# Kernel tuning notes

Hardware: AMD Instinct MI355X
Metric: run time of the kernel (lower is better)

## Reference

```python
import jax, jax.numpy as jnp
import numpy as np

B, L, D = 2, 2048, 2560
H, KV, HD = 8, 4, 256
FF = 10240
WINDOW = 1024
ROPE_BASE = 10000.0
EPS = 1e-6


def rmsnorm(x, scale=None):
    x32 = x.astype(jnp.float32)
    var = jnp.mean(jnp.square(x32), axis=-1, keepdims=True)
    xn = x32 * jax.lax.rsqrt(var + EPS)
    return xn if scale is None else xn * scale.astype(jnp.float32)


def apply_rope(x, positions, base):
    # full RoPE (rope_fraction=1.0): rotate pairs (i, i+head_dim//2)
    hd = x.shape[-1]
    half = hd // 2
    timescale = base ** (2.0 * jnp.arange(half, dtype=jnp.float32) / hd)
    ang = positions[:, :, None].astype(jnp.float32) / timescale  # [B,L,half]
    sin = jnp.sin(ang)[:, :, None, :]  # [B,L,1,half]
    cos = jnp.cos(ang)[:, :, None, :]
    x1, x2 = x[..., :half], x[..., half:]
    return jnp.concatenate([x1 * cos - x2 * sin, x2 * cos + x1 * sin], axis=-1)


def setup_inputs() -> dict:
    key = jax.random.key(0)
    ks = jax.random.split(key, 16)
    s = lambda fan_in: 1.0 / np.sqrt(fan_in)
    return {
        "x": jax.random.normal(ks[0], (B, L, D), jnp.float32),
        "positions": jnp.broadcast_to(jnp.arange(L, dtype=jnp.int32), (B, L)),
        "wq": jax.random.normal(ks[1], (D, H * HD), jnp.float32) * s(D),
        "wk": jax.random.normal(ks[2], (D, KV * HD), jnp.float32) * s(D),
        "wv": jax.random.normal(ks[3], (D, KV * HD), jnp.float32) * s(D),
        "wo": jax.random.normal(ks[4], (H * HD, D), jnp.float32) * s(H * HD),
        "q_scale": jnp.ones((HD,), jnp.float32),
        "k_scale": jnp.ones((HD,), jnp.float32),
        "pre_attn_scale": jnp.ones((D,), jnp.float32),
        "post_attn_scale": jnp.ones((D,), jnp.float32),
        "pre_ffw_scale": jnp.ones((D,), jnp.float32),
        "post_ffw_scale": jnp.ones((D,), jnp.float32),
        "w_gate": jax.random.normal(ks[5], (D, FF), jnp.float32) * s(D),
        "w_up": jax.random.normal(ks[6], (D, FF), jnp.float32) * s(D),
        "w_down": jax.random.normal(ks[7], (FF, D), jnp.float32) * s(FF),
    }


def reference(x, positions, wq, wk, wv, wo, q_scale, k_scale,
              pre_attn_scale, post_attn_scale, pre_ffw_scale, post_ffw_scale,
              w_gate, w_up, w_down):
    # --- attention sub-block ---
    h = rmsnorm(x, pre_attn_scale)
    q = (h @ wq).reshape(B, L, H, HD)
    k = (h @ wk).reshape(B, L, KV, HD)
    v = (h @ wv).reshape(B, L, KV, HD)
    q = apply_rope(rmsnorm(q, q_scale), positions, ROPE_BASE)
    k = apply_rope(rmsnorm(k, k_scale), positions, ROPE_BASE)
    v = rmsnorm(v)  # RMSNormNoScale on V
    rep = H // KV
    k = jnp.repeat(k, rep, axis=2)  # [B,L,H,HD]
    v = jnp.repeat(v, rep, axis=2)
    scores = jnp.einsum("bqhd,bkhd->bhqk", q, k)  # NOTE: no 1/sqrt(d) scaling, faithful to source
    i = jnp.arange(L)[:, None]
    j = jnp.arange(L)[None, :]
    mask = (j <= i) & (j > i - WINDOW)  # causal & sliding window
    scores = jnp.where(mask[None, None, :, :], scores, -10000.0)
    probs = jax.nn.softmax(scores.astype(jnp.float32), axis=-1)
    attn = jnp.einsum("bhqk,bkhd->bqhd", probs, v).reshape(B, L, H * HD)
    attn = attn @ wo
    x = x + rmsnorm(attn, post_attn_scale)
    # --- feedforward sub-block (GeGLU) ---
    h = rmsnorm(x, pre_ffw_scale)
    hidden = jax.nn.gelu(h @ w_gate, approximate=False) * (h @ w_up)
    ffw = hidden @ w_down
    x = x + rmsnorm(ffw, post_ffw_scale)
    return x
```

## Files before the change

kernel.cpp:

```cpp
#include <hip/hip_runtime.h>
#include <math.h>

#define DEV __device__ __forceinline__

typedef _Float16 f16;
typedef _Float16 f16x8 __attribute__((ext_vector_type(8)));
typedef _Float16 f16x4 __attribute__((ext_vector_type(4)));
typedef float f32x4 __attribute__((ext_vector_type(4)));

DEV void gload_lds16(const void* g, void* l) {
  __builtin_amdgcn_global_load_lds(
      (const __attribute__((address_space(1))) void*)g,
      (__attribute__((address_space(3))) void*)l, 16, 0, 0);
}

__global__ void transpose_w(const float* __restrict__ src, f16* __restrict__ dst,
                            int R, int C) {
  __shared__ float tile[32][33];
  int c0 = blockIdx.x * 32, r0 = blockIdx.y * 32;
  int tx = threadIdx.x, ty = threadIdx.y;
#pragma unroll
  for (int j = 0; j < 32; j += 8)
    tile[ty + j][tx] = src[(size_t)(r0 + ty + j) * C + c0 + tx];
  __syncthreads();
#pragma unroll
  for (int j = 0; j < 32; j += 8)
    dst[(size_t)(c0 + ty + j) * R + r0 + tx] = (f16)tile[tx][ty + j];
}

__global__ void rope_table_k(float* __restrict__ tab) {
  int idx = blockIdx.x * 256 + threadIdx.x;
  int pos = idx >> 7, j = idx & 127;
  float ts = powf(10000.0f, (float)j * (1.0f / 128.0f));
  float ang = (float)pos / ts;
  tab[pos * 256 + j] = sinf(ang);
  tab[pos * 256 + 128 + j] = cosf(ang);
}

__global__ __launch_bounds__(256) void rmsnorm_f32_f16(
    const float* __restrict__ in, const float* __restrict__ scale,
    f16* __restrict__ out) {
  constexpr int D = 2560, N4 = D / 4;
  const int m = blockIdx.x, tid = threadIdx.x;
  const float* row = in + (size_t)m * D;
  float vals[12];
  float ss = 0.f;
#pragma unroll
  for (int it = 0; it < 3; ++it) {
    int c4 = tid + it * 256;
    if (c4 < N4) {
      float4 v = *(const float4*)(row + c4 * 4);
      vals[it * 4 + 0] = v.x; vals[it * 4 + 1] = v.y;
      vals[it * 4 + 2] = v.z; vals[it * 4 + 3] = v.w;
      ss += v.x * v.x + v.y * v.y + v.z * v.z + v.w * v.w;
    }
  }
#pragma unroll
  for (int off = 32; off; off >>= 1) ss += __shfl_xor(ss, off, 64);
  __shared__ float red[4];
  if ((tid & 63) == 0) red[tid >> 6] = ss;
  __syncthreads();
  float rs = rsqrtf((red[0] + red[1] + red[2] + red[3]) * (1.0f / D) + 1e-6f);
#pragma unroll
  for (int it = 0; it < 3; ++it) {
    int c4 = tid + it * 256;
    if (c4 < N4) {
      float4 sc = *(const float4*)(scale + c4 * 4);
      f16x4 o;
      o[0] = (f16)(vals[it * 4 + 0] * rs * sc.x);
      o[1] = (f16)(vals[it * 4 + 1] * rs * sc.y);
      o[2] = (f16)(vals[it * 4 + 2] * rs * sc.z);
      o[3] = (f16)(vals[it * 4 + 3] * rs * sc.w);
      *(f16x4*)(out + (size_t)m * D + c4 * 4) = o;
    }
  }
}

__global__ __launch_bounds__(256) void residual_rmsnorm(
    const float* x, const f16* __restrict__ y,
    const float* __restrict__ scale, float* out) {
  constexpr int D = 2560, N4 = D / 4;
  const int m = blockIdx.x, tid = threadIdx.x;
  const f16* yr = y + (size_t)m * D;
  float yv[12];
  float ss = 0.f;
#pragma unroll
  for (int it = 0; it < 3; ++it) {
    int c4 = tid + it * 256;
    if (c4 < N4) {
      f16x4 u = *(const f16x4*)(yr + c4 * 4);
      float a = (float)u[0], b = (float)u[1], c = (float)u[2], d = (float)u[3];
      yv[it * 4 + 0] = a; yv[it * 4 + 1] = b; yv[it * 4 + 2] = c; yv[it * 4 + 3] = d;
      ss += a * a + b * b + c * c + d * d;
    }
  }
#pragma unroll
  for (int off = 32; off; off >>= 1) ss += __shfl_xor(ss, off, 64);
  __shared__ float red[4];
  if ((tid & 63) == 0) red[tid >> 6] = ss;
  __syncthreads();
  float rs = rsqrtf((red[0] + red[1] + red[2] + red[3]) * (1.0f / D) + 1e-6f);
#pragma unroll
  for (int it = 0; it < 3; ++it) {
    int c4 = tid + it * 256;
    if (c4 < N4) {
      float4 xv = *(const float4*)(x + (size_t)m * D + c4 * 4);
      float4 sc = *(const float4*)(scale + c4 * 4);
      float4 o;
      o.x = xv.x + yv[it * 4 + 0] * rs * sc.x;
      o.y = xv.y + yv[it * 4 + 1] * rs * sc.y;
      o.z = xv.z + yv[it * 4 + 2] * rs * sc.z;
      o.w = xv.w + yv[it * 4 + 3] * rs * sc.w;
      *(float4*)(out + (size_t)m * D + c4 * 4) = o;
    }
  }
}

__global__ __launch_bounds__(256) void norm_rope_k(
    const f16* __restrict__ qkv, const int* __restrict__ positions,
    const float* __restrict__ q_scale, const float* __restrict__ k_scale,
    const float* __restrict__ tab,
    f16* __restrict__ q_g, f16* __restrict__ k_g, f16* __restrict__ v_n) {
  const int m = blockIdx.x;
  const int tid = threadIdx.x, w = tid >> 6, l = tid & 63;
  const int pos = positions[m];
  const float* srow = tab + (size_t)pos * 256;
  const int c0 = l * 4;
  for (int vi = w; vi < 16; vi += 4) {
    f16x4 u = *(const f16x4*)(qkv + (size_t)m * 4096 + vi * 256 + c0);
    float x0 = (float)u[0], x1 = (float)u[1], x2 = (float)u[2], x3 = (float)u[3];
    float ss = x0 * x0 + x1 * x1 + x2 * x2 + x3 * x3;
#pragma unroll
    for (int off = 32; off; off >>= 1) ss += __shfl_xor(ss, off, 64);
    float rs = rsqrtf(ss * (1.0f / 256.0f) + 1e-6f);
    if (vi < 12) {
      const float* sc = (vi < 8) ? q_scale : k_scale;
      float4 s4 = *(const float4*)(sc + c0);
      float n0 = x0 * rs * s4.x, n1 = x1 * rs * s4.y;
      float n2 = x2 * rs * s4.z, n3 = x3 * rs * s4.w;
      float p0 = __shfl_xor(n0, 32, 64), p1 = __shfl_xor(n1, 32, 64);
      float p2 = __shfl_xor(n2, 32, 64), p3 = __shfl_xor(n3, 32, 64);
      int j0 = c0 & 127;
      float4 sn = *(const float4*)(srow + j0);
      float4 cs = *(const float4*)(srow + 128 + j0);
      float sgn = (l < 32) ? -1.0f : 1.0f;
      f16x4 o;
      o[0] = (f16)(n0 * cs.x + sgn * p0 * sn.x);
      o[1] = (f16)(n1 * cs.y + sgn * p1 * sn.y);
      o[2] = (f16)(n2 * cs.z + sgn * p2 * sn.z);
      o[3] = (f16)(n3 * cs.w + sgn * p3 * sn.w);
      if (vi < 8) *(f16x4*)(q_g + (size_t)m * 2048 + vi * 256 + c0) = o;
      else        *(f16x4*)(k_g + (size_t)m * 1024 + (vi - 8) * 256 + c0) = o;
    } else {
      f16x4 o;
      o[0] = (f16)(x0 * rs); o[1] = (f16)(x1 * rs);
      o[2] = (f16)(x2 * rs); o[3] = (f16)(x3 * rs);
      *(f16x4*)(v_n + (size_t)m * 1024 + (vi - 12) * 256 + c0) = o;
    }
  }
}

__global__ void transpose_v_k(const f16* __restrict__ v_n, f16* __restrict__ vt) {
  __shared__ f16 tile[32][33];
  int bkv = blockIdx.z;
  int b = bkv >> 2, kv = bkv & 3;
  int t0 = blockIdx.x * 32, d0 = blockIdx.y * 32;
  int tx = threadIdx.x, ty = threadIdx.y;
#pragma unroll
  for (int j = 0; j < 32; j += 8)
    tile[ty + j][tx] =
        v_n[(size_t)(b * 2048 + t0 + ty + j) * 1024 + kv * 256 + d0 + tx];
  __syncthreads();
#pragma unroll
  for (int j = 0; j < 32; j += 8)
    vt[((size_t)bkv * 256 + d0 + ty + j) * 2048 + t0 + tx] = tile[tx][ty + j];
}

template <int EPI>
__global__ __launch_bounds__(512, 2) void gemm256(
    const f16* __restrict__ A, const f16* __restrict__ BT,
    f16* __restrict__ C, const f16* __restrict__ aux, int M, int N, int K) {
  extern __shared__ __align__(16) f16 lds[];
  const int tid = threadIdx.x;
  const int w = tid >> 6, l = tid & 63;
  const int l15 = l & 15, lk = l >> 4;
  const int wm = w >> 2, wn = w & 3;

  const int gx = gridDim.x;
  const int nwg = gx * gridDim.y;
  const int orig = blockIdx.y * gx + blockIdx.x;
  const int swz = (orig & 7) * (nwg >> 3) + (orig >> 3);
  const int bn = swz % gx, bm = swz / gx;

  const int NT = K >> 6;

  const int srow = tid >> 2;
  const int sg = (tid & 3) ^ ((srow >> 1) & 3);
  const f16* pA1 = A + (size_t)(bm * 256 + srow) * K + sg * 8;
  const f16* pA2 = pA1 + (size_t)128 * K;
  const f16* pB1;
  const f16* pB2;
  if constexpr (EPI == 3) {
    pB1 = BT + (size_t)(bn * 128 + srow) * K + sg * 8;
    pB2 = aux + (size_t)(bn * 128 + srow) * K + sg * 8;
  } else {
    pB1 = BT + (size_t)(bn * 256 + srow) * K + sg * 8;
    pB2 = pB1 + (size_t)128 * K;
  }

  auto stage4 = [&](int buf, int kt) {
    const int kb = kt * 64;
    f16* base = lds + (buf << 2) * 8192 + tid * 8;
#pragma unroll
    for (int kh = 0; kh < 2; ++kh) {
      f16* dA = base + (kh << 1) * 8192;
      gload_lds16(pA1 + kb + kh * 32, dA);
      gload_lds16(pA2 + kb + kh * 32, dA + 4096);
      f16* dB = base + ((kh << 1) + 1) * 8192;
      gload_lds16(pB1 + kb + kh * 32, dB);
      gload_lds16(pB2 + kb + kh * 32, dB + 4096);
    }
  };

  const int fcol = (lk ^ ((l15 >> 1) & 3)) << 3;
  const int aoff = (wm * 128 + l15) * 32 + fcol;
  const int boff = 8192 + (wn * 64 + l15) * 32 + fcol;

  f32x4 acc[8][4] = {};

  stage4(0, 0);
  asm volatile("s_waitcnt vmcnt(0)" ::: "memory");
  __builtin_amdgcn_s_barrier();
  asm volatile("" ::: "memory");

  for (int t = 0; t < NT; ++t) {
    const int buf = t & 1;
    const f16* lb0 = lds + buf * 32768;
    const f16* lb1 = lb0 + 16384;
    f16x8 a1[4], b1[4], a2[4], a3[4], b2[4], a4[4];
#pragma unroll
    for (int i = 0; i < 4; ++i) a1[i] = *(const f16x8*)(lb0 + aoff + i * 512);
#pragma unroll
    for (int i = 0; i < 4; ++i) b1[i] = *(const f16x8*)(lb0 + boff + i * 512);
#pragma unroll
    for (int i = 0; i < 4; ++i) a2[i] = *(const f16x8*)(lb0 + aoff + (4 + i) * 512);
    if (t + 1 < NT) stage4(buf ^ 1, t + 1);
#pragma unroll
    for (int i = 0; i < 4; ++i) a3[i] = *(const f16x8*)(lb1 + aoff + i * 512);
#pragma unroll
    for (int i = 0; i < 4; ++i) b2[i] = *(const f16x8*)(lb1 + boff + i * 512);
#pragma unroll
    for (int i = 0; i < 4; ++i) a4[i] = *(const f16x8*)(lb1 + aoff + (4 + i) * 512);
    __builtin_amdgcn_s_setprio(1);
#pragma unroll
    for (int mi = 0; mi < 4; ++mi)
#pragma unroll
      for (int ni = 0; ni < 4; ++ni)
        acc[mi][ni] = __builtin_amdgcn_mfma_f32_16x16x32_f16(a1[mi], b1[ni], acc[mi][ni], 0, 0, 0);
#pragma unroll
    for (int mi = 0; mi < 4; ++mi)
#pragma unroll
      for (int ni = 0; ni < 4; ++ni)
        acc[4 + mi][ni] = __builtin_amdgcn_mfma_f32_16x16x32_f16(a2[mi], b1[ni], acc[4 + mi][ni], 0, 0, 0);
#pragma unroll
    for (int mi = 0; mi < 4; ++mi)
#pragma unroll
      for (int ni = 0; ni < 4; ++ni)
        acc[mi][ni] = __builtin_amdgcn_mfma_f32_16x16x32_f16(a3[mi], b2[ni], acc[mi][ni], 0, 0, 0);
#pragma unroll
    for (int mi = 0; mi < 4; ++mi)
#pragma unroll
      for (int ni = 0; ni < 4; ++ni)
        acc[4 + mi][ni] = __builtin_amdgcn_mfma_f32_16x16x32_f16(a4[mi], b2[ni], acc[4 + mi][ni], 0, 0, 0);
    __builtin_amdgcn_s_setprio(0);
    if (t + 1 < NT) {
      asm volatile("s_waitcnt vmcnt(0)" ::: "memory");
      __builtin_amdgcn_s_barrier();
      asm volatile("" ::: "memory");
    }
  }

  if constexpr (EPI == 3) {
    __syncthreads();
    float* xls = (float*)lds;
    if (wn < 2) {
#pragma unroll
      for (int mi = 0; mi < 8; ++mi)
#pragma unroll
        for (int ni = 0; ni < 4; ++ni)
#pragma unroll
          for (int i = 0; i < 4; ++i) {
            int row = wm * 128 + mi * 16 + lk * 4 + i;
            int col = wn * 64 + ni * 16 + l15;
            float v = acc[mi][ni][i];
            v = 0.5f * v * (1.0f + erff(v * 0.70710678118654752f));
            xls[row * 128 + col] = v;
          }
    }
    __syncthreads();
    if (wn >= 2) {
#pragma unroll
      for (int mi = 0; mi < 8; ++mi)
#pragma unroll
        for (int ni = 0; ni < 4; ++ni)
#pragma unroll
          for (int i = 0; i < 4; ++i) {
            int row = wm * 128 + mi * 16 + lk * 4 + i;
            int colg = (wn - 2) * 64 + ni * 16 + l15;
            float g = xls[row * 128 + colg];
            float v = g * acc[mi][ni][i];
            C[(size_t)(bm * 256 + row) * N + bn * 128 + colg] = (f16)v;
          }
    }
  } else {
#pragma unroll
    for (int mi = 0; mi < 8; ++mi) {
#pragma unroll
      for (int ni = 0; ni < 4; ++ni) {
#pragma unroll
        for (int i = 0; i < 4; ++i) {
          int row = bm * 256 + wm * 128 + mi * 16 + lk * 4 + i;
          int col = bn * 256 + wn * 64 + ni * 16 + l15;
          size_t idx = (size_t)row * N + col;
          float v = acc[mi][ni][i];
          if constexpr (EPI == 1) {
            v = 0.5f * v * (1.0f + erff(v * 0.70710678118654752f));
          } else if constexpr (EPI == 2) {
            v *= (float)aux[idx];
          }
          C[idx] = (f16)v;
        }
      }
    }
  }
}

__global__ __launch_bounds__(256) void flash_attn_k(
    const f16* __restrict__ q_g, const f16* __restrict__ k_g,
    const f16* __restrict__ vt, f16* __restrict__ ctx) {
  constexpr int KP = 264, VP = 40, PP = 40;
  __shared__ f16 Ks[32 * KP];
  __shared__ f16 Vs[256 * VP];
  __shared__ f16 Ps[4][16 * PP];
  const int qt = blockIdx.x, h = blockIdx.y, b = blockIdx.z;
  const int tid = threadIdx.x, w = tid >> 6, l = tid & 63;
  const int l15 = l & 15, lk = l >> 4;
  const int kv = h >> 1;

  f16x8 aq[8];
  const int qrow = qt * 64 + w * 16 + l15;
  const f16* qp = q_g + (size_t)(b * 2048 + qrow) * 2048 + h * 256 + lk * 8;
#pragma unroll
  for (int kc = 0; kc < 8; ++kc) aq[kc] = *(const f16x8*)(qp + kc * 32);

  f32x4 o[16] = {};
  float mrow[4] = {-1e30f, -1e30f, -1e30f, -1e30f};
  float lrow[4] = {0.f, 0.f, 0.f, 0.f};

  int kt_lo = 2 * qt - 32; if (kt_lo < 0) kt_lo = 0;
  const int kt_hi = 2 * qt + 1;
  const int iqb = qt * 64 + w * 16 + lk * 4;

  for (int kt = kt_lo; kt <= kt_hi; ++kt) {
    __syncthreads();
#pragma unroll
    for (int it = 0; it < 4; ++it) {
      int ch = tid + it * 256;
      int jl = ch >> 5, kcc = (ch & 31) * 8;
      *(f16x8*)&Ks[jl * KP + kcc] = *(const f16x8*)(
          k_g + (size_t)(b * 2048 + kt * 32 + jl) * 1024 + kv * 256 + kcc);
      int d = ch >> 2, tc = (ch & 3) * 8;
      *(f16x8*)&Vs[d * VP + tc] = *(const f16x8*)(
          vt + ((size_t)(b * 4 + kv) * 256 + d) * 2048 + kt * 32 + tc);
    }
    __syncthreads();
    f32x4 s[2] = {};
#pragma unroll
    for (int ct = 0; ct < 2; ++ct)
#pragma unroll
      for (int kc = 0; kc < 8; ++kc) {
        f16x8 bk = *(const f16x8*)&Ks[(ct * 16 + l15) * KP + kc * 32 + lk * 8];
        s[ct] = __builtin_amdgcn_mfma_f32_16x16x32_f16(aq[kc], bk, s[ct], 0, 0, 0);
      }
    float pm[4] = {-1e30f, -1e30f, -1e30f, -1e30f};
#pragma unroll
    for (int ct = 0; ct < 2; ++ct)
#pragma unroll
      for (int i = 0; i < 4; ++i) {
        int iq = iqb + i;
        int j = kt * 32 + ct * 16 + l15;
        bool valid = (j <= iq) && (j > iq - 1024);
        float sv = valid ? s[ct][i] : -1e30f;
        s[ct][i] = sv;
        pm[i] = fmaxf(pm[i], sv);
      }
#pragma unroll
    for (int i = 0; i < 4; ++i)
#pragma unroll
      for (int off = 1; off < 16; off <<= 1)
        pm[i] = fmaxf(pm[i], __shfl_xor(pm[i], off, 64));
    float corr[4], rsum[4];
#pragma unroll
    for (int i = 0; i < 4; ++i) {
      float mn = fmaxf(mrow[i], pm[i]);
      corr[i] = __expf(mrow[i] - mn);
      mrow[i] = mn;
      rsum[i] = 0.f;
    }
#pragma unroll
    for (int ct = 0; ct < 2; ++ct)
#pragma unroll
      for (int i = 0; i < 4; ++i) {
        float p = (s[ct][i] > -1e29f) ? __expf(s[ct][i] - mrow[i]) : 0.f;
        s[ct][i] = p;
        rsum[i] += p;
      }
#pragma unroll
    for (int i = 0; i < 4; ++i) {
#pragma unroll
      for (int off = 1; off < 16; off <<= 1) rsum[i] += __shfl_xor(rsum[i], off, 64);
      lrow[i] = lrow[i] * corr[i] + rsum[i];
    }
#pragma unroll
    for (int dt = 0; dt < 16; ++dt)
#pragma unroll
      for (int i = 0; i < 4; ++i) o[dt][i] *= corr[i];
#pragma unroll
    for (int ct = 0; ct < 2; ++ct)
#pragma unroll
      for (int i = 0; i < 4; ++i)
        Ps[w][(lk * 4 + i) * PP + ct * 16 + l15] = (f16)s[ct][i];
    __syncthreads();
    f16x8 pa = *(const f16x8*)&Ps[w][l15 * PP + lk * 8];
#pragma unroll
    for (int dt = 0; dt < 16; ++dt) {
      f16x8 bv = *(const f16x8*)&Vs[(dt * 16 + l15) * VP + lk * 8];
      o[dt] = __builtin_amdgcn_mfma_f32_16x16x32_f16(pa, bv, o[dt], 0, 0, 0);
    }
  }
  float inv[4];
#pragma unroll
  for (int i = 0; i < 4; ++i) inv[i] = 1.0f / lrow[i];
  f16* op = ctx + (size_t)(b * 2048 + qt * 64 + w * 16 + lk * 4) * 2048 + h * 256 + l15;
#pragma unroll
  for (int dt = 0; dt < 16; ++dt)
#pragma unroll
    for (int i = 0; i < 4; ++i)
      op[(size_t)i * 2048 + dt * 16] = (f16)(o[dt][i] * inv[i]);
}

extern "C" void kernel_launch(void* const* d_in, const int* in_sizes, int n_in,
                              void* d_out, int out_size, void* d_ws, size_t ws_size,
                              hipStream_t stream) {
  const float* x = (const float*)d_in[0];
  const int* positions = (const int*)d_in[1];
  const float* wq = (const float*)d_in[2];
  const float* wk = (const float*)d_in[3];
  const float* wv = (const float*)d_in[4];
  const float* wo = (const float*)d_in[5];
  const float* q_scale = (const float*)d_in[6];
  const float* k_scale = (const float*)d_in[7];
  const float* pre_attn = (const float*)d_in[8];
  const float* post_attn = (const float*)d_in[9];
  const float* pre_ffw = (const float*)d_in[10];
  const float* post_ffw = (const float*)d_in[11];
  const float* w_gate = (const float*)d_in[12];
  const float* w_up = (const float*)d_in[13];
  const float* w_down = (const float*)d_in[14];
  float* out = (float*)d_out;

  static bool s_attr = []() {
    hipFuncSetAttribute(reinterpret_cast<const void*>(&gemm256<0>),
                        hipFuncAttributeMaxDynamicSharedMemorySize, 131072);
    hipFuncSetAttribute(reinterpret_cast<const void*>(&gemm256<1>),
                        hipFuncAttributeMaxDynamicSharedMemorySize, 131072);
    hipFuncSetAttribute(reinterpret_cast<const void*>(&gemm256<2>),
                        hipFuncAttributeMaxDynamicSharedMemorySize, 131072);
    hipFuncSetAttribute(reinterpret_cast<const void*>(&gemm256<3>),
                        hipFuncAttributeMaxDynamicSharedMemorySize, 131072);
    return true;
  }();
  (void)s_attr;

  const size_t WT_BIG   = (size_t)20480 * 2560 * 2;
  const size_t WT_SMALL = (size_t)10240 * 2560 * 2;
  const size_t TAB_B = (size_t)2048 * 256 * 4;
  const size_t H_B   = (size_t)4096 * 2560 * 2;
  const size_t ACT_B = (size_t)92280832;
  auto aln = [](size_t v) { return (v + 255) & ~(size_t)255; };
  const bool big = ws_size >= aln(WT_BIG) + aln(TAB_B) + aln(H_B) + aln(ACT_B);

  char* ws = (char*)d_ws;
  size_t off = 0;
  auto alloc = [&](size_t bytes) {
    char* p = ws + off;
    off += (bytes + 255) & ~(size_t)255;
    return p;
  };
  f16* wT    = (f16*)alloc(big ? WT_BIG : WT_SMALL);
  float* tab = (float*)alloc(TAB_B);
  f16* h     = (f16*)alloc(H_B);
  char* act  = alloc(ACT_B);
  f16* qkv    = (f16*)(act);
  f16* q_g    = (f16*)(act + (size_t)33554432);
  f16* k_g    = (f16*)(act + (size_t)33554432 + 16777216);
  f16* v_n    = (f16*)(act + (size_t)33554432 + 16777216 + 8388608);
  f16* vtb    = (f16*)(act + (size_t)33554432 + 16777216 + 2 * 8388608);
  f16* ctx    = (f16*)(act + (size_t)33554432 + 16777216 + 3 * 8388608);
  f16* attn_o = (f16*)(act);
  f16* gbuf = (f16*)(act);
  f16* ffw  = h;
  f16* wuT  = wT + (size_t)10240 * 2560;
  (void)in_sizes; (void)n_in; (void)out_size;

  dim3 tb(32, 8);
  rope_table_k<<<1024, 256, 0, stream>>>(tab);

  rmsnorm_f32_f16<<<4096, 256, 0, stream>>>(x, pre_attn, h);
  transpose_w<<<dim3(2048 / 32, 2560 / 32), tb, 0, stream>>>(wq, wT, 2560, 2048);
  transpose_w<<<dim3(1024 / 32, 2560 / 32), tb, 0, stream>>>(wk, wT + (size_t)2048 * 2560, 2560, 1024);
  transpose_w<<<dim3(1024 / 32, 2560 / 32), tb, 0, stream>>>(wv, wT + (size_t)3072 * 2560, 2560, 1024);
  gemm256<0><<<dim3(4096 / 256, 4096 / 256), 512, 131072, stream>>>(h, wT, qkv, nullptr, 4096, 4096, 2560);
  norm_rope_k<<<4096, 256, 0, stream>>>(qkv, positions, q_scale, k_scale, tab, q_g, k_g, v_n);
  transpose_v_k<<<dim3(2048 / 32, 256 / 32, 8), tb, 0, stream>>>(v_n, vtb);
  flash_attn_k<<<dim3(32, 8, 2), 256, 0, stream>>>(q_g, k_g, vtb, ctx);
  transpose_w<<<dim3(2560 / 32, 2048 / 32), tb, 0, stream>>>(wo, wT, 2048, 2560);
  gemm256<0><<<dim3(2560 / 256, 4096 / 256), 512, 131072, stream>>>(ctx, wT, attn_o, nullptr, 4096, 2560, 2048);
  residual_rmsnorm<<<4096, 256, 0, stream>>>(x, attn_o, post_attn, out);

  rmsnorm_f32_f16<<<4096, 256, 0, stream>>>(out, pre_ffw, h);
  if (big) {
    transpose_w<<<dim3(10240 / 32, 2560 / 32), tb, 0, stream>>>(w_gate, wT, 2560, 10240);
    transpose_w<<<dim3(10240 / 32, 2560 / 32), tb, 0, stream>>>(w_up, wuT, 2560, 10240);
    gemm256<3><<<dim3(80, 16), 512, 131072, stream>>>(h, wT, gbuf, wuT, 4096, 10240, 2560);
  } else {
    transpose_w<<<dim3(10240 / 32, 2560 / 32), tb, 0, stream>>>(w_gate, wT, 2560, 10240);
    gemm256<1><<<dim3(10240 / 256, 4096 / 256), 512, 131072, stream>>>(h, wT, gbuf, nullptr, 4096, 10240, 2560);
    transpose_w<<<dim3(10240 / 32, 2560 / 32), tb, 0, stream>>>(w_up, wT, 2560, 10240);
    gemm256<2><<<dim3(10240 / 256, 4096 / 256), 512, 131072, stream>>>(h, wT, gbuf, gbuf, 4096, 10240, 2560);
  }
  transpose_w<<<dim3(2560 / 32, 10240 / 32), tb, 0, stream>>>(w_down, wT, 10240, 2560);
  gemm256<0><<<dim3(2560 / 256, 4096 / 256), 512, 131072, stream>>>(gbuf, wT, ffw, nullptr, 4096, 2560, 10240);
  residual_rmsnorm<<<4096, 256, 0, stream>>>(out, ffw, post_ffw, out);
}
```

Baseline: 1.259 ms.

## Split GEMM K-tile staging into half-tile groups with finer-grained vmcnt waits

Restructures the GEMM main loop so each 64-wide K tile is consumed in two 32-wide halves, with a barrier between them. Global-to-LDS loads for the next tile are issued piecewise between MFMA groups, and the tile after that is prefetched into the freed half-buffer. Partial vmcnt waits replace full drains, so memory traffic overlaps compute more evenly. The GeGLU epilogue also stores the gelu intermediate as f16 with a padded row stride, which cuts LDS footprint and bank conflicts but adds an extra barrier per tile and a small precision loss.

```diff
diff --git a/kernel.cpp b/kernel.cpp
--- a/kernel.cpp
+++ b/kernel.cpp
@@ -208,18 +208,13 @@
     pB2 = pB1 + (size_t)128 * K;
   }
 
-  auto stage4 = [&](int buf, int kt) {
-    const int kb = kt * 64;
-    f16* base = lds + (buf << 2) * 8192 + tid * 8;
-#pragma unroll
-    for (int kh = 0; kh < 2; ++kh) {
-      f16* dA = base + (kh << 1) * 8192;
-      gload_lds16(pA1 + kb + kh * 32, dA);
-      gload_lds16(pA2 + kb + kh * 32, dA + 4096);
-      f16* dB = base + ((kh << 1) + 1) * 8192;
-      gload_lds16(pB1 + kb + kh * 32, dB);
-      gload_lds16(pB2 + kb + kh * 32, dB + 4096);
-    }
+  auto stage = [&](int op, int kh, int buf, int kt) {
+    const int kb = kt * 64 + kh * 32;
+    const f16* s1 = (op ? pB1 : pA1) + kb;
+    const f16* s2 = (op ? pB2 : pA2) + kb;
+    f16* dst = lds + ((buf << 2) + (kh << 1) + op) * 8192 + tid * 8;
+    gload_lds16(s1, dst);
+    gload_lds16(s2, dst + 4096);
   };
 
   const int fcol = (lk ^ ((l15 >> 1) & 3)) << 3;
@@ -228,61 +223,84 @@
 
   f32x4 acc[8][4] = {};
 
-  stage4(0, 0);
-  asm volatile("s_waitcnt vmcnt(0)" ::: "memory");
+  stage(0, 0, 0, 0);
+  stage(1, 0, 0, 0);
+  stage(0, 1, 0, 0);
+  stage(1, 1, 0, 0);
+  if (NT > 1) stage(0, 0, 1, 1);
+  asm volatile("s_waitcnt vmcnt(6)" ::: "memory");
   __builtin_amdgcn_s_barrier();
   asm volatile("" ::: "memory");
 
   for (int t = 0; t < NT; ++t) {
-    const int buf = t & 1;
+    const int buf = t & 1, nbuf = buf ^ 1;
     const f16* lb0 = lds + buf * 32768;
     const f16* lb1 = lb0 + 16384;
-    f16x8 a1[4], b1[4], a2[4], a3[4], b2[4], a4[4];
-#pragma unroll
-    for (int i = 0; i < 4; ++i) a1[i] = *(const f16x8*)(lb0 + aoff + i * 512);
-#pragma unroll
-    for (int i = 0; i < 4; ++i) b1[i] = *(const f16x8*)(lb0 + boff + i * 512);
-#pragma unroll
-    for (int i = 0; i < 4; ++i) a2[i] = *(const f16x8*)(lb0 + aoff + (4 + i) * 512);
-    if (t + 1 < NT) stage4(buf ^ 1, t + 1);
-#pragma unroll
-    for (int i = 0; i < 4; ++i) a3[i] = *(const f16x8*)(lb1 + aoff + i * 512);
-#pragma unroll
-    for (int i = 0; i < 4; ++i) b2[i] = *(const f16x8*)(lb1 + boff + i * 512);
-#pragma unroll
-    for (int i = 0; i < 4; ++i) a4[i] = *(const f16x8*)(lb1 + aoff + (4 + i) * 512);
-    __builtin_amdgcn_s_setprio(1);
-#pragma unroll
-    for (int mi = 0; mi < 4; ++mi)
-#pragma unroll
-      for (int ni = 0; ni < 4; ++ni)
-        acc[mi][ni] = __builtin_amdgcn_mfma_f32_16x16x32_f16(a1[mi], b1[ni], acc[mi][ni], 0, 0, 0);
-#pragma unroll
-    for (int mi = 0; mi < 4; ++mi)
-#pragma unroll
-      for (int ni = 0; ni < 4; ++ni)
-        acc[4 + mi][ni] = __builtin_amdgcn_mfma_f32_16x16x32_f16(a2[mi], b1[ni], acc[4 + mi][ni], 0, 0, 0);
-#pragma unroll
-    for (int mi = 0; mi < 4; ++mi)
-#pragma unroll
-      for (int ni = 0; ni < 4; ++ni)
-        acc[mi][ni] = __builtin_amdgcn_mfma_f32_16x16x32_f16(a3[mi], b2[ni], acc[mi][ni], 0, 0, 0);
-#pragma unroll
-    for (int mi = 0; mi < 4; ++mi)
-#pragma unroll
-      for (int ni = 0; ni < 4; ++ni)
-        acc[4 + mi][ni] = __builtin_amdgcn_mfma_f32_16x16x32_f16(a4[mi], b2[ni], acc[4 + mi][ni], 0, 0, 0);
-    __builtin_amdgcn_s_setprio(0);
-    if (t + 1 < NT) {
-      asm volatile("s_waitcnt vmcnt(0)" ::: "memory");
-      __builtin_amdgcn_s_barrier();
-      asm volatile("" ::: "memory");
-    }
+    {
+      f16x8 a1[4], b[4], a2[4];
+#pragma unroll
+      for (int i = 0; i < 4; ++i) a1[i] = *(const f16x8*)(lb0 + aoff + i * 512);
+#pragma unroll
+      for (int i = 0; i < 4; ++i) b[i] = *(const f16x8*)(lb0 + boff + i * 512);
+#pragma unroll
+      for (int i = 0; i < 4; ++i) a2[i] = *(const f16x8*)(lb0 + aoff + (4 + i) * 512);
+      if (t + 1 < NT) stage(1, 0, nbuf, t + 1);
+      __builtin_amdgcn_s_setprio(1);
+#pragma unroll
+      for (int mi = 0; mi < 4; ++mi)
+#pragma unroll
+        for (int ni = 0; ni < 4; ++ni)
+          acc[mi][ni] = __builtin_amdgcn_mfma_f32_16x16x32_f16(a1[mi], b[ni], acc[mi][ni], 0, 0, 0);
+      __builtin_amdgcn_s_setprio(0);
+      if (t + 1 < NT) stage(0, 1, nbuf, t + 1);
+      __builtin_amdgcn_s_setprio(1);
+#pragma unroll
+      for (int mi = 0; mi < 4; ++mi)
+#pragma unroll
+        for (int ni = 0; ni < 4; ++ni)
+          acc[4 + mi][ni] = __builtin_amdgcn_mfma_f32_16x16x32_f16(a2[mi], b[ni], acc[4 + mi][ni], 0, 0, 0);
+      __builtin_amdgcn_s_setprio(0);
+    }
+    if (t + 1 < NT) asm volatile("s_waitcnt vmcnt(6)" ::: "memory");
+    else            asm volatile("s_waitcnt vmcnt(0)" ::: "memory");
+    __builtin_amdgcn_s_barrier();
+    asm volatile("" ::: "memory");
+    {
+      f16x8 a1[4], b[4], a2[4];
+#pragma unroll
+      for (int i = 0; i < 4; ++i) a1[i] = *(const f16x8*)(lb1 + aoff + i * 512);
+#pragma unroll
+      for (int i = 0; i < 4; ++i) b[i] = *(const f16x8*)(lb1 + boff + i * 512);
+#pragma unroll
+      for (int i = 0; i < 4; ++i) a2[i] = *(const f16x8*)(lb1 + aoff + (4 + i) * 512);
+      if (t + 1 < NT) stage(1, 1, nbuf, t + 1);
+      __builtin_amdgcn_s_setprio(1);
+#pragma unroll
+      for (int mi = 0; mi < 4; ++mi)
+#pragma unroll
+        for (int ni = 0; ni < 4; ++ni)
+          acc[mi][ni] = __builtin_amdgcn_mfma_f32_16x16x32_f16(a1[mi], b[ni], acc[mi][ni], 0, 0, 0);
+      __builtin_amdgcn_s_setprio(0);
+      if (t + 2 < NT) stage(0, 0, buf, t + 2);
+      __builtin_amdgcn_s_setprio(1);
+#pragma unroll
+      for (int mi = 0; mi < 4; ++mi)
+#pragma unroll
+        for (int ni = 0; ni < 4; ++ni)
+          acc[4 + mi][ni] = __builtin_amdgcn_mfma_f32_16x16x32_f16(a2[mi], b[ni], acc[4 + mi][ni], 0, 0, 0);
+      __builtin_amdgcn_s_setprio(0);
+    }
+    if (t + 2 < NT)      asm volatile("s_waitcnt vmcnt(6)" ::: "memory");
+    else if (t + 1 < NT) asm volatile("s_waitcnt vmcnt(4)" ::: "memory");
+    else                 asm volatile("s_waitcnt vmcnt(0)" ::: "memory");
+    __builtin_amdgcn_s_barrier();
+    asm volatile("" ::: "memory");
   }
 
   if constexpr (EPI == 3) {
+    constexpr int XP = 136;
     __syncthreads();
-    float* xls = (float*)lds;
+    f16* xls = lds;
     if (wn < 2) {
 #pragma unroll
       for (int mi = 0; mi < 8; ++mi)
@@ -294,7 +312,7 @@
             int col = wn * 64 + ni * 16 + l15;
             float v = acc[mi][ni][i];
             v = 0.5f * v * (1.0f + erff(v * 0.70710678118654752f));
-            xls[row * 128 + col] = v;
+            xls[row * XP + col] = (f16)v;
           }
     }
     __syncthreads();
@@ -307,7 +325,7 @@
           for (int i = 0; i < 4; ++i) {
             int row = wm * 128 + mi * 16 + lk * 4 + i;
             int colg = (wn - 2) * 64 + ni * 16 + l15;
-            float g = xls[row * 128 + colg];
+            float g = (float)xls[row * XP + colg];
             float v = g * acc[mi][ni][i];
             C[(size_t)(bm * 256 + row) * N + bn * 128 + colg] = (f16)v;
           }
```

New measurement: 1.198 ms. 1.05x faster.
